# Kernel optimization log

Measured on AMD Instinct MI355X. Metric: run time of the kernel, lower is better.

The kernel has to match this reference:

```python
import jax, jax.numpy as jnp
import numpy as np

B = 65536
IN_F = 512
OUT_F = 256
NUM_GROUPS = 8
EPS = 1e-5


def setup_inputs() -> dict:
    key = jax.random.key(0)
    ks = jax.random.split(key, 6)
    return {
        "x": jax.random.normal(ks[0], (B, IN_F), dtype=jnp.float32),
        "weight": jax.random.normal(ks[1], (OUT_F, IN_F), dtype=jnp.float32) * 0.05,
        "bias_linear": jax.random.normal(ks[2], (OUT_F,), dtype=jnp.float32) * 0.05,
        "weight_gn": jax.random.normal(ks[3], (OUT_F,), dtype=jnp.float32),
        "bias_gn": jax.random.normal(ks[4], (OUT_F,), dtype=jnp.float32),
        "bias": jax.random.normal(ks[5], (1, OUT_F, 1, 1), dtype=jnp.float32),
    }


def reference(x, weight, bias_linear, weight_gn, bias_gn, bias):
    # Linear: (B, IN_F) @ (IN_F, OUT_F) + bias -> (B, OUT_F)
    h = jnp.einsum("bi,oi->bo", x, weight) + bias_linear
    # GroupNorm over channel dim (dim=1) with NUM_GROUPS groups
    g = h.reshape(B, NUM_GROUPS, OUT_F // NUM_GROUPS)
    mean = jnp.mean(g, axis=2, keepdims=True)
    var = jnp.mean(jnp.square(g - mean), axis=2, keepdims=True)
    gn = ((g - mean) * jax.lax.rsqrt(var + EPS)).reshape(B, OUT_F)
    gn = gn * weight_gn + bias_gn
    # Min over channels, keepdim -> (B, 1)
    min_vals = jnp.min(gn, axis=1, keepdims=True)
    # torch broadcasting: (B,1) + (1,256,1,1) -> (1,256,B,1)
    result = min_vals + bias
    return result
```

## Files before the change

kernel.cpp:

```cpp
#include <hip/hip_runtime.h>
#include <hip/hip_bf16.h>

#define B_ROWS 65536
#define K_DIM  512
#define N_DIM  256
#define EPS    1e-5f
#define MTILE  64
#define LDS_STRIDE 264

using short8  = __attribute__((ext_vector_type(8))) short;
using floatx4 = __attribute__((ext_vector_type(4))) float;

__device__ __forceinline__ unsigned short f2bf(float f) {
    unsigned u = __builtin_bit_cast(unsigned, f);
    u += 0x7FFFu + ((u >> 16) & 1u);
    return (unsigned short)(u >> 16);
}

__global__ __launch_bounds__(64) void pack_w(const float* __restrict__ W,
                                             unsigned short* __restrict__ P) {
    int b    = blockIdx.x;
    int nt   = b >> 4, kk = b & 15;
    int lane = threadIdx.x;
    int l15  = lane & 15, quad = lane >> 4;
    const float* src = W + (size_t)(nt * 16 + l15) * K_DIM + kk * 32 + quad * 8;
    short8 v;
#pragma unroll
    for (int j = 0; j < 8; ++j) v[j] = (short)f2bf(src[j]);
    *(short8*)(P + ((size_t)(nt * 16 + kk) * 64 + lane) * 8) = v;
}

__global__ __launch_bounds__(256) void gemm_gn_min(
    const float* __restrict__ X, const unsigned short* __restrict__ P,
    const float* __restrict__ bias_lin, const float* __restrict__ wgn,
    const float* __restrict__ bgn, float* __restrict__ Mout)
{
    __shared__ unsigned short Ash[MTILE * LDS_STRIDE];
    __shared__ float sm_min[4][MTILE];

    const int tid  = threadIdx.x;
    const int wave = tid >> 6, lane = tid & 63;
    const int l15  = lane & 15, quad = lane >> 4;
    const size_t row0 = (size_t)blockIdx.x * MTILE;

    floatx4 acc[4][4] = {};

    for (int kh = 0; kh < 2; ++kh) {
        if (kh) __syncthreads();
        for (int i = tid; i < MTILE * 64; i += 256) {
            int r = i >> 6, c4 = (i & 63) << 2;
            const float4 f = *(const float4*)(X + (row0 + r) * K_DIM + kh * 256 + c4);
            ushort4 h;
            h.x = f2bf(f.x); h.y = f2bf(f.y); h.z = f2bf(f.z); h.w = f2bf(f.w);
            *(ushort4*)(&Ash[r * LDS_STRIDE + c4]) = h;
        }
        __syncthreads();

#pragma unroll
        for (int kk = 0; kk < 8; ++kk) {
            const int kkg = kh * 8 + kk;
            short8 a[4], b[4];
#pragma unroll
            for (int rt = 0; rt < 4; ++rt)
                a[rt] = *(const short8*)&Ash[(rt * 16 + l15) * LDS_STRIDE + kk * 32 + quad * 8];
#pragma unroll
            for (int ct = 0; ct < 4; ++ct) {
                int nt = wave * 4 + ct;
                b[ct] = *(const short8*)(P + (((size_t)nt * 16 + kkg) * 64 + lane) * 8);
            }
#pragma unroll
            for (int rt = 0; rt < 4; ++rt)
#pragma unroll
                for (int ct = 0; ct < 4; ++ct)
                    acc[rt][ct] = __builtin_amdgcn_mfma_f32_16x16x32_bf16(
                        a[rt], b[ct], acc[rt][ct], 0, 0, 0);
        }
    }

    float bl[4], wg[4], bg[4];
#pragma unroll
    for (int ct = 0; ct < 4; ++ct) {
        int col = wave * 64 + ct * 16 + l15;
        bl[ct] = bias_lin[col]; wg[ct] = wgn[col]; bg[ct] = bgn[col];
    }

#pragma unroll
    for (int rt = 0; rt < 4; ++rt) {
#pragma unroll
        for (int reg = 0; reg < 4; ++reg) {
            float v[4];
#pragma unroll
            for (int ct = 0; ct < 4; ++ct) v[ct] = acc[rt][ct][reg] + bl[ct];
            float rmin = 1e30f;
#pragma unroll
            for (int h = 0; h < 2; ++h) {
                float va = v[2 * h], vb = v[2 * h + 1];
                float s = va + vb, ss = va * va + vb * vb;
#pragma unroll
                for (int m = 1; m < 16; m <<= 1) {
                    s  += __shfl_xor(s, m);
                    ss += __shfl_xor(ss, m);
                }
                float mean = s * (1.0f / 32.0f);
                float var  = ss * (1.0f / 32.0f) - mean * mean;
                float inv  = rsqrtf(var + EPS);
                float ga = (va - mean) * inv * wg[2 * h]     + bg[2 * h];
                float gb = (vb - mean) * inv * wg[2 * h + 1] + bg[2 * h + 1];
                float mn = fminf(ga, gb);
#pragma unroll
                for (int m = 1; m < 16; m <<= 1) mn = fminf(mn, __shfl_xor(mn, m));
                rmin = fminf(rmin, mn);
            }
            if (l15 == 0) sm_min[wave][rt * 16 + quad * 4 + reg] = rmin;
        }
    }
    __syncthreads();
    if (tid < MTILE) {
        float m0 = fminf(fminf(sm_min[0][tid], sm_min[1][tid]),
                         fminf(sm_min[2][tid], sm_min[3][tid]));
        Mout[row0 + tid] = m0;
    }
}

__global__ __launch_bounds__(256) void bcast(const float* __restrict__ Mv,
                                             const float* __restrict__ bias,
                                             float* __restrict__ out) {
    const int c  = blockIdx.y;
    const int b0 = (blockIdx.x * 256 + threadIdx.x) * 4;
    const float bc = bias[c];
    float4 m = *(const float4*)(Mv + b0);
    float4 o;
    o.x = m.x + bc; o.y = m.y + bc; o.z = m.z + bc; o.w = m.w + bc;
    *(float4*)(out + (size_t)c * B_ROWS + b0) = o;
}

extern "C" void kernel_launch(void* const* d_in, const int* in_sizes, int n_in,
                              void* d_out, int out_size, void* d_ws, size_t ws_size,
                              hipStream_t stream) {
    const float* x    = (const float*)d_in[0];
    const float* w    = (const float*)d_in[1];
    const float* bl   = (const float*)d_in[2];
    const float* wg   = (const float*)d_in[3];
    const float* bg   = (const float*)d_in[4];
    const float* bias = (const float*)d_in[5];

    unsigned short* P  = (unsigned short*)d_ws;
    float*          Mv = (float*)((char*)d_ws + 256 * 1024);
    float*          out = (float*)d_out;

    hipLaunchKernelGGL(pack_w, dim3(256), dim3(64), 0, stream, w, P);
    hipLaunchKernelGGL(gemm_gn_min, dim3(B_ROWS / MTILE), dim3(256), 0, stream,
                       x, P, bl, wg, bg, Mv);
    hipLaunchKernelGGL(bcast, dim3(B_ROWS / 1024, N_DIM), dim3(256), 0, stream,
                       Mv, bias, out);
}
```

Measured before the change: 253.9 us.

## Fuse broadcast into GEMM-GroupNorm-min kernel and halve row tile

Folds the separate broadcast kernel into the GEMM/GroupNorm/min kernel: each block writes its 32 row minima plus the per-channel bias for all 256 channels directly to the output. This removes one kernel launch and the round trip of the min vector through global memory. The row tile shrinks from 64 to 32 and launch bounds request 6 blocks per CU, which doubles the grid and raises occupancy. In exchange the packed weights are re-read twice as often, and each block's output stores are short 128-byte segments scattered across channel rows.

```diff
diff --git a/kernel.cpp b/kernel.cpp
--- a/kernel.cpp
+++ b/kernel.cpp
@@ -5,7 +5,7 @@
 #define K_DIM  512
 #define N_DIM  256
 #define EPS    1e-5f
-#define MTILE  64
+#define MTILE  32
 #define LDS_STRIDE 264
 
 using short8  = __attribute__((ext_vector_type(8))) short;
@@ -30,20 +30,22 @@
     *(short8*)(P + ((size_t)(nt * 16 + kk) * 64 + lane) * 8) = v;
 }
 
-__global__ __launch_bounds__(256) void gemm_gn_min(
+__global__ __launch_bounds__(256, 6) void gemm_gn_min_bcast(
     const float* __restrict__ X, const unsigned short* __restrict__ P,
     const float* __restrict__ bias_lin, const float* __restrict__ wgn,
-    const float* __restrict__ bgn, float* __restrict__ Mout)
+    const float* __restrict__ bgn, const float* __restrict__ bias,
+    float* __restrict__ out)
 {
     __shared__ unsigned short Ash[MTILE * LDS_STRIDE];
     __shared__ float sm_min[4][MTILE];
+    __shared__ float m_sh[MTILE];
 
     const int tid  = threadIdx.x;
     const int wave = tid >> 6, lane = tid & 63;
     const int l15  = lane & 15, quad = lane >> 4;
     const size_t row0 = (size_t)blockIdx.x * MTILE;
 
-    floatx4 acc[4][4] = {};
+    floatx4 acc[2][4] = {};
 
     for (int kh = 0; kh < 2; ++kh) {
         if (kh) __syncthreads();
@@ -59,9 +61,9 @@
 #pragma unroll
         for (int kk = 0; kk < 8; ++kk) {
             const int kkg = kh * 8 + kk;
-            short8 a[4], b[4];
+            short8 a[2], b[4];
 #pragma unroll
-            for (int rt = 0; rt < 4; ++rt)
+            for (int rt = 0; rt < 2; ++rt)
                 a[rt] = *(const short8*)&Ash[(rt * 16 + l15) * LDS_STRIDE + kk * 32 + quad * 8];
 #pragma unroll
             for (int ct = 0; ct < 4; ++ct) {
@@ -69,7 +71,7 @@
                 b[ct] = *(const short8*)(P + (((size_t)nt * 16 + kkg) * 64 + lane) * 8);
             }
 #pragma unroll
-            for (int rt = 0; rt < 4; ++rt)
+            for (int rt = 0; rt < 2; ++rt)
 #pragma unroll
                 for (int ct = 0; ct < 4; ++ct)
                     acc[rt][ct] = __builtin_amdgcn_mfma_f32_16x16x32_bf16(
@@ -85,7 +87,7 @@
     }
 
 #pragma unroll
-    for (int rt = 0; rt < 4; ++rt) {
+    for (int rt = 0; rt < 2; ++rt) {
 #pragma unroll
         for (int reg = 0; reg < 4; ++reg) {
             float v[4];
@@ -115,23 +117,21 @@
         }
     }
     __syncthreads();
-    if (tid < MTILE) {
-        float m0 = fminf(fminf(sm_min[0][tid], sm_min[1][tid]),
-                         fminf(sm_min[2][tid], sm_min[3][tid]));
-        Mout[row0 + tid] = m0;
+    if (tid < MTILE)
+        m_sh[tid] = fminf(fminf(sm_min[0][tid], sm_min[1][tid]),
+                          fminf(sm_min[2][tid], sm_min[3][tid]));
+    __syncthreads();
+
+    const int lane8 = tid & 7, cgrp = tid >> 3;
+    float4 mv = *(const float4*)&m_sh[lane8 * 4];
+#pragma unroll
+    for (int pass = 0; pass < 8; ++pass) {
+        int c = pass * 32 + cgrp;
+        float bc = bias[c];
+        float4 o;
+        o.x = mv.x + bc; o.y = mv.y + bc; o.z = mv.z + bc; o.w = mv.w + bc;
+        *(float4*)(out + (size_t)c * B_ROWS + row0 + lane8 * 4) = o;
     }
-}
-
-__global__ __launch_bounds__(256) void bcast(const float* __restrict__ Mv,
-                                             const float* __restrict__ bias,
-                                             float* __restrict__ out) {
-    const int c  = blockIdx.y;
-    const int b0 = (blockIdx.x * 256 + threadIdx.x) * 4;
-    const float bc = bias[c];
-    float4 m = *(const float4*)(Mv + b0);
-    float4 o;
-    o.x = m.x + bc; o.y = m.y + bc; o.z = m.z + bc; o.w = m.w + bc;
-    *(float4*)(out + (size_t)c * B_ROWS + b0) = o;
 }
 
 extern "C" void kernel_launch(void* const* d_in, const int* in_sizes, int n_in,
@@ -144,13 +144,10 @@
     const float* bg   = (const float*)d_in[4];
     const float* bias = (const float*)d_in[5];
 
-    unsigned short* P  = (unsigned short*)d_ws;
-    float*          Mv = (float*)((char*)d_ws + 256 * 1024);
-    float*          out = (float*)d_out;
+    unsigned short* P = (unsigned short*)d_ws;
+    float* out = (float*)d_out;
 
     hipLaunchKernelGGL(pack_w, dim3(256), dim3(64), 0, stream, w, P);
-    hipLaunchKernelGGL(gemm_gn_min, dim3(B_ROWS / MTILE), dim3(256), 0, stream,
-                       x, P, bl, wg, bg, Mv);
-    hipLaunchKernelGGL(bcast, dim3(B_ROWS / 1024, N_DIM), dim3(256), 0, stream,
-                       Mv, bias, out);
+    hipLaunchKernelGGL(gemm_gn_min_bcast, dim3(B_ROWS / MTILE), dim3(256), 0, stream,
+                       x, P, bl, wg, bg, bias, out);
 }
```

After: 260.2 us. +2.5%, slower.
